# Kernel tuning notes

Measured on AMD Instinct MI355X. Metric: run time of the kernel, lower is better.

Reference implementation:

```python
import jax, jax.numpy as jnp
import numpy as np

B, T, D, H = 2, 2048, 1024, 16
DH = D // H


def setup_inputs() -> dict:
    key = jax.random.key(0)
    ks = jax.random.split(key, 8)
    s = 1.0 / np.sqrt(D)  # xavier-ish scale
    return {
        "query": jax.random.normal(ks[0], (B, T, D), jnp.float32),
        "key": jax.random.normal(ks[1], (B, T, D), jnp.float32),
        "value": jax.random.normal(ks[2], (B, T, D), jnp.float32),
        "Wq": jax.random.normal(ks[3], (D, D), jnp.float32) * s,
        "bq": jnp.zeros((D,), jnp.float32),
        "Wk": jax.random.normal(ks[4], (D, D), jnp.float32) * s,
        "bk": jnp.zeros((D,), jnp.float32),
        "Wv": jax.random.normal(ks[5], (D, D), jnp.float32) * s,
        "bv": jnp.zeros((D,), jnp.float32),
        "Wo": jax.random.normal(ks[6], (D, D), jnp.float32) * s,
        "bo": jnp.zeros((D,), jnp.float32),
        # causal mask (B, T, T); True = attend
        "mask": jnp.broadcast_to(jnp.tril(jnp.ones((T, T), bool)), (B, T, T)),
    }


def _split_heads(x):  # (B, T, D) -> (B, H, T, Dh)
    return x.reshape(B, T, H, DH).transpose(0, 2, 1, 3)


def reference(query, key, value, Wq, bq, Wk, bk, Wv, bv, Wo, bo, mask):
    q = _split_heads(query @ Wq + bq)
    k = _split_heads(key @ Wk + bk)
    v = _split_heads(value @ Wv + bv)
    scores = jnp.einsum("bhqd,bhkd->bhqk", q, k) / jnp.sqrt(jnp.float32(DH))
    scores = jnp.where(mask[:, None, :, :], scores, -jnp.inf)
    w = jax.nn.softmax(scores, axis=-1)
    out = jnp.einsum("bhqk,bhkd->bhqd", w, v)
    out = out.transpose(0, 2, 1, 3).reshape(B, T, D)  # merge heads
    return out @ Wo + bo
```

## Files before the change

kernel.cpp:

```cpp
#include <hip/hip_runtime.h>

typedef unsigned short u16;
typedef __attribute__((ext_vector_type(4))) float f32x4;
typedef __attribute__((ext_vector_type(8))) short bf16x8;

#define MFMA16(a,b,c) __builtin_amdgcn_mfma_f32_16x16x32_bf16((a),(b),(c),0,0,0)

__device__ inline u16 f2bf(float f){
  union { float f; unsigned u; } v; v.f = f;
  unsigned r = v.u + 0x7FFFu + ((v.u >> 16) & 1u);
  return (u16)(r >> 16);
}
__device__ inline u16 f2bf_fast(float f){
  union { float f; unsigned u; } v; v.f = f;
  return (u16)((v.u + 0x8000u) >> 16);
}
__device__ inline unsigned pk2bf(float x, float y){
  union { float f; unsigned u; } a, b; a.f=x; b.f=y;
  return ((a.u + 0x8000u)>>16) | ((b.u + 0x8000u) & 0xFFFF0000u);
}

typedef const __attribute__((address_space(1))) unsigned int* gas_ptr;
typedef __attribute__((address_space(3))) unsigned int* las_ptr;
__device__ inline void gload_lds16(const u16* g, u16* l){
  __builtin_amdgcn_global_load_lds((gas_ptr)(const void*)g, (las_ptr)(void*)l, 16, 0, 0);
}

struct CvtArgs { const float* x[3]; u16* y[3]; };
__global__ void k_cvt3(CvtArgs a, int n4){
  const float* x = a.x[blockIdx.y];
  u16* y = a.y[blockIdx.y];
  int i = blockIdx.x*blockDim.x + threadIdx.x;
  if (i < n4){
    float4 v = ((const float4*)x)[i];
    ushort4 o;
    o.x = f2bf(v.x); o.y = f2bf(v.y); o.z = f2bf(v.z); o.w = f2bf(v.w);
    ((ushort4*)y)[i] = o;
  }
}

struct TwbArgs { const float* W[4]; u16* Wt[4]; };
__global__ void k_twb4(TwbArgs a){
  __shared__ u16 t[32][33];
  const float* W = a.W[blockIdx.z];
  u16* Wt = a.Wt[blockIdx.z];
  int kb = blockIdx.x*32, nb = blockIdx.y*32;
  int tx = threadIdx.x, ty = threadIdx.y;
  #pragma unroll
  for (int i=0;i<32;i+=8)
    t[ty+i][tx] = f2bf(W[(size_t)(kb+ty+i)*1024 + nb+tx]);
  __syncthreads();
  #pragma unroll
  for (int i=0;i<32;i+=8)
    Wt[(size_t)(nb+ty+i)*1024 + kb+tx] = t[tx][ty+i];
}

__global__ void k_tv(const u16* __restrict__ V, u16* __restrict__ VT){
  __shared__ u16 t[32][33];
  int tb = blockIdx.x*32;
  int db = blockIdx.y*32;
  int bh = blockIdx.z;
  int b = bh>>4, h = bh&15;
  int tx = threadIdx.x, ty = threadIdx.y;
  #pragma unroll
  for (int i=0;i<32;i+=8)
    t[ty+i][tx] = V[(size_t)(b*2048 + tb+ty+i)*1024 + h*64 + db+tx];
  __syncthreads();
  #pragma unroll
  for (int i=0;i<32;i+=8)
    VT[(size_t)(bh*64 + db+ty+i)*2048 + tb+tx] = t[tx][ty+i];
}

struct GemmArgs3 { const u16* A[3]; const u16* Bt[3]; const float* bias[3]; u16* C[3]; };

#define STAGE_A(slot, kh) { \
  int c0_ = tid, c1_ = tid + 512; \
  gload_lds16(A + (size_t)(row0 + (c0_>>2))*1024 + (kh)*32 + (((c0_&3) ^ ((c0_>>3)&3))*8), &As[slot][c0_*8]); \
  gload_lds16(A + (size_t)(row0 + (c1_>>2))*1024 + (kh)*32 + (((c1_&3) ^ ((c1_>>3)&3))*8), &As[slot][c1_*8]); }
#define STAGE_B(slot, kh) { \
  int c0_ = tid, c1_ = tid + 512; \
  gload_lds16(Bt + (size_t)(col0 + (c0_>>2))*1024 + (kh)*32 + (((c0_&3) ^ ((c0_>>3)&3))*8), &Bs[slot][c0_*8]); \
  gload_lds16(Bt + (size_t)(col0 + (c1_>>2))*1024 + (kh)*32 + (((c1_&3) ^ ((c1_>>3)&3))*8), &Bs[slot][c1_*8]); }

#define KHALF_BODY(s) { \
  const u16* Al = &As[s][0]; const u16* Bl = &Bs[s][0]; \
  bf16x8 bfr[4], af[4]; \
  _Pragma("unroll") \
  for (int nf=0;nf<4;nf++) \
    bfr[nf] = *(const bf16x8*)(Bl + (wc*64+nf*16+lo)*32 + pg*8); \
  _Pragma("unroll") \
  for (int mf=0;mf<4;mf++) \
    af[mf] = *(const bf16x8*)(Al + (wr*128+mf*16+lo)*32 + pg*8); \
  __builtin_amdgcn_s_setprio(1); \
  _Pragma("unroll") \
  for (int mf=0;mf<4;mf++) \
    _Pragma("unroll") \
    for (int nf=0;nf<4;nf++) \
      acc[mf][nf] = MFMA16(af[mf], bfr[nf], acc[mf][nf]); \
  __builtin_amdgcn_s_setprio(0); \
  STAGE_B_GUARDED \
  _Pragma("unroll") \
  for (int mf=0;mf<4;mf++) \
    af[mf] = *(const bf16x8*)(Al + (wr*128+(mf+4)*16+lo)*32 + pg*8); \
  __builtin_amdgcn_s_setprio(1); \
  _Pragma("unroll") \
  for (int mf=0;mf<4;mf++) \
    _Pragma("unroll") \
    for (int nf=0;nf<4;nf++) \
      acc[mf+4][nf] = MFMA16(af[mf], bfr[nf], acc[mf+4][nf]); \
  __builtin_amdgcn_s_setprio(0); }

__global__ __launch_bounds__(512) void k_gemm3(GemmArgs3 g){
  const int N=1024;
  __shared__ __attribute__((aligned(16))) u16 As[4][256*32];
  __shared__ __attribute__((aligned(16))) u16 Bs[4][256*32];
  int flat = blockIdx.x;
  int swz = (flat&7)*24 + (flat>>3);
  int bz = swz>>6, rem = swz&63;
  int bx = rem>>2, by = rem&3;
  const u16* A = g.A[bz]; const u16* Bt = g.Bt[bz];
  const float* bias = g.bias[bz]; u16* C = g.C[bz];
  const int tid = threadIdx.x;
  const int wave = tid>>6, lane = tid&63;
  const int lo = lane&15, hi = lane>>4;
  const int wr = wave>>2, wc = wave&3;
  const int row0 = bx*256, col0 = by*256;
  const int pg = hi ^ ((lo>>1)&3);

  f32x4 acc[8][4];
  #pragma unroll
  for (int i=0;i<8;i++)
    #pragma unroll
    for (int j=0;j<4;j++) acc[i][j] = (f32x4){0.f,0.f,0.f,0.f};

  STAGE_A(0,0); STAGE_B(0,0);
  STAGE_A(1,1); STAGE_B(1,1);
  STAGE_A(2,2); STAGE_B(2,2);

  for (int h = 0; h < 29; ++h){
    const int s = h & 3;
    STAGE_A((h+3)&3, h+3);
    asm volatile("s_waitcnt vmcnt(10)" ::: "memory");
    __builtin_amdgcn_s_barrier();
    #define STAGE_B_GUARDED STAGE_B((h+3)&3, h+3);
    KHALF_BODY(s)
    #undef STAGE_B_GUARDED
  }
  {
    asm volatile("s_waitcnt vmcnt(8)" ::: "memory");
    __builtin_amdgcn_s_barrier();
    #define STAGE_B_GUARDED
    KHALF_BODY(29&3)
    #undef STAGE_B_GUARDED
  }
  {
    asm volatile("s_waitcnt vmcnt(4)" ::: "memory");
    __builtin_amdgcn_s_barrier();
    #define STAGE_B_GUARDED
    KHALF_BODY(30&3)
    #undef STAGE_B_GUARDED
  }
  {
    asm volatile("s_waitcnt vmcnt(0)" ::: "memory");
    __builtin_amdgcn_s_barrier();
    #define STAGE_B_GUARDED
    KHALF_BODY(31&3)
    #undef STAGE_B_GUARDED
  }

  #pragma unroll
  for (int mf=0;mf<8;mf++){
    #pragma unroll
    for (int nf=0;nf<4;nf++){
      int r0 = row0 + wr*128 + mf*16 + hi*4;
      int c0 = col0 + wc*64 + nf*16 + lo;
      float bv = bias[c0];
      #pragma unroll
      for (int r=0;r<4;r++)
        C[(size_t)(r0+r)*N + c0] = f2bf(acc[mf][nf][r] + bv);
    }
  }
}

__global__ __launch_bounds__(256) void k_gemmO(const u16* __restrict__ A, const u16* __restrict__ Bt,
                                               const float* __restrict__ bias, float* __restrict__ C){
  const int N=1024, K=1024;
  int f = blockIdx.x;
  int xcd = f & 7, idx = f >> 3;
  int bx = xcd*8 + (idx>>3), by = idx & 7;
  __shared__ __attribute__((aligned(16))) u16 As[64*64];
  __shared__ __attribute__((aligned(16))) u16 Bs[128*64];
  const int tid  = threadIdx.x;
  const int wave = tid>>6, lane = tid&63;
  const int lo = lane&15, hi = lane>>4;
  const int row0 = bx*64, col0 = by*128;
  const int wm = (wave>>1)*32, wn = (wave&1)*64;
  f32x4 acc[2][4];
  #pragma unroll
  for (int i=0;i<2;i++)
    #pragma unroll
    for (int j=0;j<4;j++) acc[i][j] = (f32x4){0.f,0.f,0.f,0.f};

  for (int k0=0; k0<K; k0+=64){
    #pragma unroll
    for (int r=0;r<2;r++){
      int c = r*256 + tid;
      gload_lds16(A + (size_t)(row0 + (c>>3))*K + k0 + (c&7)*8, As + c*8);
    }
    #pragma unroll
    for (int r=0;r<4;r++){
      int c = r*256 + tid;
      gload_lds16(Bt + (size_t)(col0 + (c>>3))*K + k0 + (c&7)*8, Bs + c*8);
    }
    __syncthreads();
    __builtin_amdgcn_s_setprio(1);
    #pragma unroll
    for (int ks=0;ks<2;ks++){
      bf16x8 af[2], bfr[4];
      #pragma unroll
      for (int mf=0;mf<2;mf++)
        af[mf] = *(const bf16x8*)(As + (wm+mf*16+lo)*64 + ks*32 + hi*8);
      #pragma unroll
      for (int nf=0;nf<4;nf++)
        bfr[nf] = *(const bf16x8*)(Bs + (wn+nf*16+lo)*64 + ks*32 + hi*8);
      #pragma unroll
      for (int mf=0;mf<2;mf++)
        #pragma unroll
        for (int nf=0;nf<4;nf++)
          acc[mf][nf] = MFMA16(af[mf], bfr[nf], acc[mf][nf]);
    }
    __builtin_amdgcn_s_setprio(0);
    __syncthreads();
  }
  #pragma unroll
  for (int mf=0;mf<2;mf++){
    #pragma unroll
    for (int nf=0;nf<4;nf++){
      int r0 = row0 + wm + mf*16 + hi*4;
      int c0 = col0 + wn + nf*16 + lo;
      float bv = bias[c0];
      #pragma unroll
      for (int r=0;r<4;r++)
        C[(size_t)(r0+r)*N + c0] = acc[mf][nf][r] + bv;
    }
  }
}

__global__ __launch_bounds__(256) void k_attn(
    const u16* __restrict__ Q, const u16* __restrict__ Kp,
    const u16* __restrict__ VT, u16* __restrict__ O)
{
  const int T=2048, D=1024;
  __shared__ __attribute__((aligned(16))) u16 Ks[2][64*64];
  __shared__ __attribute__((aligned(16))) u16 Vs[2][64*64];
  __shared__ __attribute__((aligned(16))) u16 Plds[4][16*64];
  int f = blockIdx.x + (blockIdx.y<<5);
  int xcd = f & 7, idx = f >> 3;
  const int bh = (xcd<<2) | (idx&3);
  const int qb = 31 - (idx>>2);
  const int b = bh>>4, h = bh&15;
  const int tid = threadIdx.x;
  const int wave = tid>>6, lane = tid&63;
  const int lo = lane&15, hi = lane>>4;
  const int wi = wave>>1, wj = wave&1;
  const int lo7 = lo&7;
  const float NEG = -1e30f;
  const float sc = 0.125f * 1.44269504f;
  const float MC = 64.0f * sc;
  const bf16x8 ones = {0x3F80,0x3F80,0x3F80,0x3F80,0x3F80,0x3F80,0x3F80,0x3F80};

  const int c0 = tid, c1 = 256 + tid;
  const int sr0 = c0>>3, sj0 = (c0&7)^(sr0&7);
  const int sr1 = c1>>3, sj1 = (c1&7)^(sr1&7);
  const u16* Kbase = Kp + (size_t)(b*T)*D + h*64;
  const u16* Vbase = VT + (size_t)(bh*64)*T;
  const size_t kOff0 = (size_t)sr0*D + sj0*8, kOff1 = (size_t)sr1*D + sj1*8;
  const size_t vOff0 = (size_t)sr0*T + sj0*8, vOff1 = (size_t)sr1*T + sj1*8;

  const int qrow0 = qb*64 + wi*32;
  bf16x8 qf[2][2];
  #pragma unroll
  for (int qnf=0;qnf<2;qnf++){
    const u16* Qr = Q + (size_t)(b*T + qrow0 + qnf*16 + lo)*D + h*64;
    qf[qnf][0] = *(const bf16x8*)(Qr + hi*8);
    qf[qnf][1] = *(const bf16x8*)(Qr + 32 + hi*8);
  }

  f32x4 o[2][4];
  #pragma unroll
  for (int i=0;i<2;i++)
    #pragma unroll
    for (int j=0;j<4;j++) o[i][j] = (f32x4){0.f,0.f,0.f,0.f};
  f32x4 lac[2];
  lac[0] = (f32x4){0.f,0.f,0.f,0.f};
  lac[1] = (f32x4){0.f,0.f,0.f,0.f};

  gload_lds16(Kbase + kOff0, &Ks[0][c0*8]);
  gload_lds16(Kbase + kOff1, &Ks[0][c1*8]);
  gload_lds16(Vbase + vOff0, &Vs[0][c0*8]);
  gload_lds16(Vbase + vOff1, &Vs[0][c1*8]);
  __syncthreads();

  u16* Pl = &Plds[wave][0];
  const int kcof0 = ((     hi) ^ lo7)*8;
  const int kcof1 = (( 4 + hi) ^ lo7)*8;
  const int vcof  = ((wj*4+hi) ^ lo7)*8;

  int cur = 0;
  for (int kb=0; kb<=qb; kb++){
    if (kb < qb){
      const u16* Kt = Kbase + (size_t)(kb+1)*64*D;
      const u16* Vt = Vbase + (kb+1)*64;
      gload_lds16(Kt + kOff0, &Ks[cur^1][c0*8]);
      gload_lds16(Kt + kOff1, &Ks[cur^1][c1*8]);
      gload_lds16(Vt + vOff0, &Vs[cur^1][c0*8]);
      gload_lds16(Vt + vOff1, &Vs[cur^1][c1*8]);
    }
    const u16* Kl = Ks[cur];
    const u16* Vl = Vs[cur];
    f32x4 s[2][2];
    __builtin_amdgcn_s_setprio(1);
    #pragma unroll
    for (int knf=0;knf<2;knf++){
      int krow = wj*32 + knf*16 + lo;
      bf16x8 kf0 = *(const bf16x8*)(Kl + krow*64 + kcof0);
      bf16x8 kf1 = *(const bf16x8*)(Kl + krow*64 + kcof1);
      #pragma unroll
      for (int qnf=0;qnf<2;qnf++){
        f32x4 z = (f32x4){0.f,0.f,0.f,0.f};
        z = MFMA16(kf0, qf[qnf][0], z);
        s[knf][qnf] = MFMA16(kf1, qf[qnf][1], z);
      }
    }
    __builtin_amdgcn_s_setprio(0);
    if (kb == qb){
      int ql = wi*32 + lo;
      #pragma unroll
      for (int knf=0;knf<2;knf++){
        int kl0 = wj*32 + knf*16 + 4*hi;
        #pragma unroll
        for (int qnf=0;qnf<2;qnf++){
          int qv = ql + qnf*16;
          #pragma unroll
          for (int r=0;r<4;r++)
            if (kl0 + r > qv) s[knf][qnf][r] = NEG;
        }
      }
    }
    #pragma unroll
    for (int knf=0;knf<2;knf++)
      #pragma unroll
      for (int qnf=0;qnf<2;qnf++){
        float p0 = __builtin_amdgcn_exp2f(__builtin_fmaf(s[knf][qnf][0], sc, -MC));
        float p1 = __builtin_amdgcn_exp2f(__builtin_fmaf(s[knf][qnf][1], sc, -MC));
        float p2 = __builtin_amdgcn_exp2f(__builtin_fmaf(s[knf][qnf][2], sc, -MC));
        float p3 = __builtin_amdgcn_exp2f(__builtin_fmaf(s[knf][qnf][3], sc, -MC));
        unsigned w0 = pk2bf(p0, p1);
        unsigned w1 = pk2bf(p2, p3);
        int gphys = (qnf*4 + knf*2 + (hi>>1)) ^ lo7;
        uint2 wv; wv.x = w0; wv.y = w1;
        *(uint2*)&Pl[lo*64 + gphys*8 + 4*(hi&1)] = wv;
      }
    bf16x8 pa0 = *(const bf16x8*)&Pl[lo*64 + kcof0];
    bf16x8 pa1 = *(const bf16x8*)&Pl[lo*64 + kcof1];
    __builtin_amdgcn_s_setprio(1);
    lac[0] = MFMA16(pa0, ones, lac[0]);
    lac[1] = MFMA16(pa1, ones, lac[1]);
    #pragma unroll
    for (int dhnf=0;dhnf<4;dhnf++){
      bf16x8 vf = *(const bf16x8*)(Vl + (dhnf*16+lo)*64 + vcof);
      o[0][dhnf] = MFMA16(pa0, vf, o[0][dhnf]);
      o[1][dhnf] = MFMA16(pa1, vf, o[1][dhnf]);
    }
    __builtin_amdgcn_s_setprio(0);
    __syncthreads();
    cur ^= 1;
  }
  float* os  = (float*)&Ks[0][0];
  float* lsc = (float*)&Vs[0][0];
  if (wj == 1){
    #pragma unroll
    for (int qnf=0;qnf<2;qnf++){
      #pragma unroll
      for (int dhnf=0;dhnf<4;dhnf++)
        #pragma unroll
        for (int r=0;r<4;r++)
          os[((wi*32 + qnf*16 + 4*hi + r)<<6) + dhnf*16 + lo] = o[qnf][dhnf][r];
      if (lo == 0)
        #pragma unroll
        for (int r=0;r<4;r++)
          lsc[wi*32 + qnf*16 + 4*hi + r] = lac[qnf][r];
    }
  }
  __syncthreads();
  if (wj == 0){
    #pragma unroll
    for (int qnf=0;qnf<2;qnf++)
      #pragma unroll
      for (int r=0;r<4;r++){
        int qloc = wi*32 + qnf*16 + 4*hi + r;
        float lt = lac[qnf][r] + lsc[qloc];
        float rinv = 1.0f / lt;
        #pragma unroll
        for (int dhnf=0;dhnf<4;dhnf++){
          float val = o[qnf][dhnf][r] + os[(qloc<<6) + dhnf*16 + lo];
          O[(size_t)(b*T + qb*64 + qloc)*D + h*64 + dhnf*16 + lo] = f2bf_fast(val * rinv);
        }
      }
  }
}

extern "C" void kernel_launch(void* const* d_in, const int* in_sizes, int n_in,
                              void* d_out, int out_size, void* d_ws, size_t ws_size,
                              hipStream_t stream) {
  const int B=2, T=2048, D=1024;
  const int M = B*T;
  const float* query = (const float*)d_in[0];
  const float* key   = (const float*)d_in[1];
  const float* value = (const float*)d_in[2];
  const float* Wq = (const float*)d_in[3];  const float* bq = (const float*)d_in[4];
  const float* Wk = (const float*)d_in[5];  const float* bk = (const float*)d_in[6];
  const float* Wv = (const float*)d_in[7];  const float* bv = (const float*)d_in[8];
  const float* Wo = (const float*)d_in[9];  const float* bo = (const float*)d_in[10];
  float* out = (float*)d_out;

  char* ws = (char*)d_ws;
  const size_t MB = 1024*1024;
  u16* xq  = (u16*)(ws + 0*MB);
  u16* xk  = (u16*)(ws + 8*MB);
  u16* xv  = (u16*)(ws + 16*MB);
  u16* WqT = (u16*)(ws + 24*MB);
  u16* WkT = (u16*)(ws + 26*MB);
  u16* WvT = (u16*)(ws + 28*MB);
  u16* WoT = (u16*)(ws + 30*MB);
  u16* Qp  = (u16*)(ws + 32*MB);
  u16* Kp  = (u16*)(ws + 40*MB);
  u16* Vp  = (u16*)(ws + 48*MB);
  u16* VTp = (u16*)(ws + 56*MB);
  u16* AO  = (u16*)(ws + 64*MB);

  int n4 = M*D/4;
  CvtArgs ca; ca.x[0]=query; ca.x[1]=key; ca.x[2]=value; ca.y[0]=xq; ca.y[1]=xk; ca.y[2]=xv;
  k_cvt3<<<dim3(n4/256, 3), 256, 0, stream>>>(ca, n4);

  TwbArgs ta; ta.W[0]=Wq; ta.W[1]=Wk; ta.W[2]=Wv; ta.W[3]=Wo;
  ta.Wt[0]=WqT; ta.Wt[1]=WkT; ta.Wt[2]=WvT; ta.Wt[3]=WoT;
  k_twb4<<<dim3(32,32,4), dim3(32,8), 0, stream>>>(ta);

  GemmArgs3 ga;
  ga.A[0]=xq; ga.A[1]=xk; ga.A[2]=xv;
  ga.Bt[0]=WqT; ga.Bt[1]=WkT; ga.Bt[2]=WvT;
  ga.bias[0]=bq; ga.bias[1]=bk; ga.bias[2]=bv;
  ga.C[0]=Qp; ga.C[1]=Kp; ga.C[2]=Vp;
  k_gemm3<<<192, 512, 0, stream>>>(ga);

  k_tv<<<dim3(T/32, 2, 32), dim3(32,8), 0, stream>>>(Vp, VTp);
  k_attn<<<dim3(32,32), 256, 0, stream>>>(Qp, Kp, VTp, AO);
  k_gemmO<<<512, 256, 0, stream>>>(AO, WoT, bo, out);
}
```

Baseline: 116.5 us.

## Merge prep kernels and restructure QKV GEMM into barrier-separated phases

Fuses the input fp32-to-bf16 conversion and the weight transpose-convert into one launch, removing one kernel launch and its tail. The QKV GEMM main loop is reorganized into two phases per k-step. Each phase issues LDS fragment reads and the next global-to-LDS stage, then hits a workgroup barrier and an lgkmcnt wait before running its MFMA burst. This is meant to keep the waves in lockstep so loads and MFMAs interleave, at the cost of more barriers per iteration.

Result: faster. 113.3 us (median of 3 runs) (-2.7%).

```diff
diff --git a/kernel.cpp b/kernel.cpp
--- a/kernel.cpp
+++ b/kernel.cpp
@@ -26,33 +26,34 @@
   __builtin_amdgcn_global_load_lds((gas_ptr)(const void*)g, (las_ptr)(void*)l, 16, 0, 0);
 }
 
-struct CvtArgs { const float* x[3]; u16* y[3]; };
-__global__ void k_cvt3(CvtArgs a, int n4){
-  const float* x = a.x[blockIdx.y];
-  u16* y = a.y[blockIdx.y];
-  int i = blockIdx.x*blockDim.x + threadIdx.x;
-  if (i < n4){
-    float4 v = ((const float4*)x)[i];
+struct PrepArgs { const float* x[3]; u16* y[3]; const float* W[4]; u16* Wt[4]; };
+__global__ void k_prep(PrepArgs a){
+  __shared__ u16 t[32][33];
+  int blk = blockIdx.x;
+  int tid = threadIdx.x;
+  if (blk < 12288){
+    int tn = blk >> 12;
+    int i  = (blk & 4095)*256 + tid;
+    float4 v = ((const float4*)a.x[tn])[i];
     ushort4 o;
     o.x = f2bf(v.x); o.y = f2bf(v.y); o.z = f2bf(v.z); o.w = f2bf(v.w);
-    ((ushort4*)y)[i] = o;
-  }
-}
-
-struct TwbArgs { const float* W[4]; u16* Wt[4]; };
-__global__ void k_twb4(TwbArgs a){
-  __shared__ u16 t[32][33];
-  const float* W = a.W[blockIdx.z];
-  u16* Wt = a.Wt[blockIdx.z];
-  int kb = blockIdx.x*32, nb = blockIdx.y*32;
-  int tx = threadIdx.x, ty = threadIdx.y;
-  #pragma unroll
-  for (int i=0;i<32;i+=8)
-    t[ty+i][tx] = f2bf(W[(size_t)(kb+ty+i)*1024 + nb+tx]);
-  __syncthreads();
-  #pragma unroll
-  for (int i=0;i<32;i+=8)
-    Wt[(size_t)(nb+ty+i)*1024 + kb+tx] = t[tx][ty+i];
+    ((ushort4*)a.y[tn])[i] = o;
+  } else {
+    int w = blk - 12288;
+    int z = w >> 10;
+    int xy = w & 1023;
+    int kb = (xy & 31)*32, nb = (xy >> 5)*32;
+    const float* W = a.W[z];
+    u16* Wt = a.Wt[z];
+    int tx = tid & 31, ty = tid >> 5;
+    #pragma unroll
+    for (int i=0;i<32;i+=8)
+      t[ty+i][tx] = f2bf(W[(size_t)(kb+ty+i)*1024 + nb+tx]);
+    __syncthreads();
+    #pragma unroll
+    for (int i=0;i<32;i+=8)
+      Wt[(size_t)(nb+ty+i)*1024 + kb+tx] = t[tx][ty+i];
+  }
 }
 
 __global__ void k_tv(const u16* __restrict__ V, u16* __restrict__ VT){
@@ -82,15 +83,17 @@
   gload_lds16(Bt + (size_t)(col0 + (c0_>>2))*1024 + (kh)*32 + (((c0_&3) ^ ((c0_>>3)&3))*8), &Bs[slot][c0_*8]); \
   gload_lds16(Bt + (size_t)(col0 + (c1_>>2))*1024 + (kh)*32 + (((c1_&3) ^ ((c1_>>3)&3))*8), &Bs[slot][c1_*8]); }
 
-#define KHALF_BODY(s) { \
+#define PHASE1(s, STAGE_STMT) { \
   const u16* Al = &As[s][0]; const u16* Bl = &Bs[s][0]; \
-  bf16x8 bfr[4], af[4]; \
   _Pragma("unroll") \
   for (int nf=0;nf<4;nf++) \
     bfr[nf] = *(const bf16x8*)(Bl + (wc*64+nf*16+lo)*32 + pg*8); \
   _Pragma("unroll") \
   for (int mf=0;mf<4;mf++) \
     af[mf] = *(const bf16x8*)(Al + (wr*128+mf*16+lo)*32 + pg*8); \
+  STAGE_STMT \
+  __builtin_amdgcn_s_barrier(); \
+  asm volatile("s_waitcnt lgkmcnt(0)" ::: "memory"); \
   __builtin_amdgcn_s_setprio(1); \
   _Pragma("unroll") \
   for (int mf=0;mf<4;mf++) \
@@ -98,17 +101,25 @@
     for (int nf=0;nf<4;nf++) \
       acc[mf][nf] = MFMA16(af[mf], bfr[nf], acc[mf][nf]); \
   __builtin_amdgcn_s_setprio(0); \
-  STAGE_B_GUARDED \
+  __builtin_amdgcn_s_barrier(); }
+
+#define PHASE2(s, STAGE_STMT, VM_STMT) { \
+  const u16* Al = &As[s][0]; \
   _Pragma("unroll") \
   for (int mf=0;mf<4;mf++) \
     af[mf] = *(const bf16x8*)(Al + (wr*128+(mf+4)*16+lo)*32 + pg*8); \
+  STAGE_STMT \
+  VM_STMT \
+  __builtin_amdgcn_s_barrier(); \
+  asm volatile("s_waitcnt lgkmcnt(0)" ::: "memory"); \
   __builtin_amdgcn_s_setprio(1); \
   _Pragma("unroll") \
   for (int mf=0;mf<4;mf++) \
     _Pragma("unroll") \
     for (int nf=0;nf<4;nf++) \
       acc[mf+4][nf] = MFMA16(af[mf], bfr[nf], acc[mf+4][nf]); \
-  __builtin_amdgcn_s_setprio(0); }
+  __builtin_amdgcn_s_setprio(0); \
+  __builtin_amdgcn_s_barrier(); }
 
 __global__ __launch_bounds__(512) void k_gemm3(GemmArgs3 g){
   const int N=1024;
@@ -136,37 +147,22 @@
   STAGE_A(0,0); STAGE_B(0,0);
   STAGE_A(1,1); STAGE_B(1,1);
   STAGE_A(2,2); STAGE_B(2,2);
-
+  asm volatile("s_waitcnt vmcnt(8)" ::: "memory");
+  __builtin_amdgcn_s_barrier();
+
+  bf16x8 bfr[4], af[4];
   for (int h = 0; h < 29; ++h){
     const int s = h & 3;
-    STAGE_A((h+3)&3, h+3);
-    asm volatile("s_waitcnt vmcnt(10)" ::: "memory");
-    __builtin_amdgcn_s_barrier();
-    #define STAGE_B_GUARDED STAGE_B((h+3)&3, h+3);
-    KHALF_BODY(s)
-    #undef STAGE_B_GUARDED
-  }
-  {
-    asm volatile("s_waitcnt vmcnt(8)" ::: "memory");
-    __builtin_amdgcn_s_barrier();
-    #define STAGE_B_GUARDED
-    KHALF_BODY(29&3)
-    #undef STAGE_B_GUARDED
-  }
-  {
-    asm volatile("s_waitcnt vmcnt(4)" ::: "memory");
-    __builtin_amdgcn_s_barrier();
-    #define STAGE_B_GUARDED
-    KHALF_BODY(30&3)
-    #undef STAGE_B_GUARDED
-  }
-  {
-    asm volatile("s_waitcnt vmcnt(0)" ::: "memory");
-    __builtin_amdgcn_s_barrier();
-    #define STAGE_B_GUARDED
-    KHALF_BODY(31&3)
-    #undef STAGE_B_GUARDED
-  }
+    const int s3 = (h+3) & 3;
+    PHASE1(s, STAGE_A(s3, h+3);)
+    PHASE2(s, STAGE_B(s3, h+3);, asm volatile("s_waitcnt vmcnt(8)" ::: "memory");)
+  }
+  PHASE1(1, )
+  PHASE2(1, , asm volatile("s_waitcnt vmcnt(4)" ::: "memory");)
+  PHASE1(2, )
+  PHASE2(2, , asm volatile("s_waitcnt vmcnt(0)" ::: "memory");)
+  PHASE1(3, )
+  PHASE2(3, , )
 
   #pragma unroll
   for (int mf=0;mf<8;mf++){
@@ -439,13 +435,12 @@
   u16* VTp = (u16*)(ws + 56*MB);
   u16* AO  = (u16*)(ws + 64*MB);
 
-  int n4 = M*D/4;
-  CvtArgs ca; ca.x[0]=query; ca.x[1]=key; ca.x[2]=value; ca.y[0]=xq; ca.y[1]=xk; ca.y[2]=xv;
-  k_cvt3<<<dim3(n4/256, 3), 256, 0, stream>>>(ca, n4);
-
-  TwbArgs ta; ta.W[0]=Wq; ta.W[1]=Wk; ta.W[2]=Wv; ta.W[3]=Wo;
-  ta.Wt[0]=WqT; ta.Wt[1]=WkT; ta.Wt[2]=WvT; ta.Wt[3]=WoT;
-  k_twb4<<<dim3(32,32,4), dim3(32,8), 0, stream>>>(ta);
+  PrepArgs pa;
+  pa.x[0]=query; pa.x[1]=key; pa.x[2]=value;
+  pa.y[0]=xq; pa.y[1]=xk; pa.y[2]=xv;
+  pa.W[0]=Wq; pa.W[1]=Wk; pa.W[2]=Wv; pa.W[3]=Wo;
+  pa.Wt[0]=WqT; pa.Wt[1]=WkT; pa.Wt[2]=WvT; pa.Wt[3]=WoT;
+  k_prep<<<16384, 256, 0, stream>>>(pa);
 
   GemmArgs3 ga;
   ga.A[0]=xq; ga.A[1]=xk; ga.A[2]=xv;
```
